# Kernel optimization log

Hardware: AMD Instinct MI355X
Metric: run time of the kernel (lower is better)

Reference implementation:

```python
import jax, jax.numpy as jnp
import numpy as np


def setup_inputs() -> dict:
    key = jax.random.key(0)
    k1, k2 = jax.random.split(key)
    BN, C, P, K = 1024, 3, 128, 15
    patches = jax.random.normal(k1, (BN, C, P, P), dtype=jnp.float32)
    kernels = jax.random.normal(k2, (BN, C, K, K), dtype=jnp.float32)
    return {
        "patches": patches,
        "kernels": kernels,
        "kernel_size": K,
        "patch_size": P,
        "fft_size": 256,  # unused by the spatial-domain path, kept for interface parity
    }


def reference(patches, kernels, kernel_size, patch_size, fft_size):
    # patches: [BN, C, P, P], kernels: [BN, C, K, K] (C == C_k branch of original)
    BN, C, P, _ = patches.shape
    K = kernel_size
    pad = K // 2
    # torch flips the kernel then runs correlation (F.conv2d) -> true convolution
    kf = jnp.flip(kernels, axis=(-2, -1))
    x = patches.reshape(1, BN * C, P, P)          # one big grouped conv
    w = kf.reshape(BN * C, 1, K, K)               # OIHW, one filter per group
    y = jax.lax.conv_general_dilated(
        x, w,
        window_strides=(1, 1),
        padding=[(pad, pad), (pad, pad)],          # zero pad == F.pad + valid conv
        dimension_numbers=("NCHW", "OIHW", "NCHW"),
        feature_group_count=BN * C,
    )
    return y.reshape(BN, C, P, P)
```

## Files before the change

### kernel.cpp

```cpp
#include <hip/hip_runtime.h>


namespace {

constexpr int P      = 128;
constexpr int K      = 15;
constexpr int HALF   = 64;
constexpr int LROWS  = HALF + K - 1;
constexpr int LM     = 36;
constexpr int LWP    = 160;
constexpr int NT     = 256;

__device__ __forceinline__ int dein(int m) {
    return (m >> 1) + (m & 1) * 20;
}

__device__ __forceinline__ int rowkey(int row) {
    return (row >> 1) & 6;
}

__global__ __launch_bounds__(NT, 3)
void dwconv_kernel(const float* __restrict__ patches,
                   const float* __restrict__ kernels,
                   float* __restrict__ out)
{
    __shared__ float xs[LROWS * LWP];

    const int tid   = threadIdx.x;
    const int n     = blockIdx.x >> 1;
    const int halfb = blockIdx.x & 1;
    const int ibase = halfb * HALF;

    const float* img  = patches + (size_t)n * (P * P);
    const float* kern = kernels + (size_t)n * (K * K);

    for (int idx = tid; idx < LROWS * LM; idx += NT) {
        const int row = idx / LM;
        const int m   = idx - row * LM;
        const int r   = ibase - 7 + row;
        const int g0  = m * 4 - 8;
        float4 v = make_float4(0.f, 0.f, 0.f, 0.f);
        if ((unsigned)r < (unsigned)P) {
            if (g0 >= 0 && g0 + 3 < P) {
                v = *reinterpret_cast<const float4*>(img + r * P + g0);
            } else {
                float t0 = 0.f, t1 = 0.f, t2 = 0.f, t3 = 0.f;
                const float* rp = img + r * P;
                if ((unsigned)(g0 + 0) < (unsigned)P) t0 = rp[g0 + 0];
                if ((unsigned)(g0 + 1) < (unsigned)P) t1 = rp[g0 + 1];
                if ((unsigned)(g0 + 2) < (unsigned)P) t2 = rp[g0 + 2];
                if ((unsigned)(g0 + 3) < (unsigned)P) t3 = rp[g0 + 3];
                v = make_float4(t0, t1, t2, t3);
            }
        }
        const int phys = dein(m) ^ rowkey(row);
        *reinterpret_cast<float4*>(xs + row * LWP + 4 * phys) = v;
    }
    __syncthreads();

    const int ty = tid >> 4;
    const int tx = tid & 15;
    const int i0 = ty * 4;
    const int j0 = tx * 8;

    const int dbase[6] = { tx + 0, tx + 20, tx + 1, tx + 21, tx + 2, tx + 22 };

    float acc[4][8];
    #pragma unroll
    for (int rr = 0; rr < 4; ++rr)
        #pragma unroll
        for (int s = 0; s < 8; ++s)
            acc[rr][s] = 0.0f;

    float xw[24];
    float kr[4][K];

    auto loadx = [&](int t) {
        const int lrow = i0 + t;
        const float* xrow = xs + lrow * LWP;
        const int key = rowkey(lrow);
        #pragma unroll
        for (int q = 0; q < 6; ++q) {
            const float4 xv =
                *reinterpret_cast<const float4*>(xrow + 4 * (dbase[q] ^ key));
            xw[q * 4 + 0] = xv.x;
            xw[q * 4 + 1] = xv.y;
            xw[q * 4 + 2] = xv.z;
            xw[q * 4 + 3] = xv.w;
        }
    };

    auto loadk = [&](int slot, int a) {
        #pragma unroll
        for (int b = 0; b < K; ++b) kr[slot][b] = kern[a * K + b];
    };

    auto fmarow = [&](int rr, int slot) {
        #pragma unroll
        for (int b = 0; b < K; ++b)
            #pragma unroll
            for (int s = 0; s < 8; ++s)
                acc[rr][s] = fmaf(xw[s + 15 - b], kr[slot][b], acc[rr][s]);
    };

    loadk(2, 14); loadk(1, 13); loadk(0, 12);
    loadx(0); fmarow(0, 2);
    loadx(1); fmarow(0, 1); fmarow(1, 2);
    loadx(2); fmarow(0, 0); fmarow(1, 1); fmarow(2, 2);

    #pragma unroll 1
    for (int tb = 3; tb <= 14; tb += 4) {
        loadk(3, 14 - tb); loadx(tb + 0);
        fmarow(0, 3); fmarow(1, 0); fmarow(2, 1); fmarow(3, 2);

        loadk(2, 13 - tb); loadx(tb + 1);
        fmarow(0, 2); fmarow(1, 3); fmarow(2, 0); fmarow(3, 1);

        loadk(1, 12 - tb); loadx(tb + 2);
        fmarow(0, 1); fmarow(1, 2); fmarow(2, 3); fmarow(3, 0);

        loadk(0, 11 - tb); loadx(tb + 3);
        fmarow(0, 0); fmarow(1, 1); fmarow(2, 2); fmarow(3, 3);
    }

    loadx(15); fmarow(1, 0); fmarow(2, 1); fmarow(3, 2);
    loadx(16); fmarow(2, 0); fmarow(3, 1);
    loadx(17); fmarow(3, 0);

    float* orow = out + (size_t)n * (P * P) + (size_t)(ibase + i0) * P + j0;
    #pragma unroll
    for (int rr = 0; rr < 4; ++rr) {
        *reinterpret_cast<float4*>(orow + rr * P + 0) =
            make_float4(acc[rr][0], acc[rr][1], acc[rr][2], acc[rr][3]);
        *reinterpret_cast<float4*>(orow + rr * P + 4) =
            make_float4(acc[rr][4], acc[rr][5], acc[rr][6], acc[rr][7]);
    }
}

}

extern "C" void kernel_launch(void* const* d_in, const int* in_sizes, int n_in,
                              void* d_out, int out_size, void* d_ws, size_t ws_size,
                              hipStream_t stream) {
    const float* patches = (const float*)d_in[0];
    const float* kernels = (const float*)d_in[1];
    float* out = (float*)d_out;

    const int n_images = in_sizes[0] / (P * P);
    const int grid = n_images * 2;

    dwconv_kernel<<<grid, NT, 0, stream>>>(patches, kernels, out);
}
```

Baseline: 490.0 us.

## Double-buffer shared-memory row loads and drop XOR swizzle for padded stride

Replaces the XOR row swizzle with a padded row stride (152 floats) to avoid LDS bank conflicts more cheaply. It double-buffers the per-row input window (xwA/xwB), so the next row's LDS loads are issued before the current row's FMAs, hiding LDS latency. The global-to-shared fill loop also swaps per-iteration division for incremental index updates. The extra 24-float buffer raises register pressure, which could cut occupancy under launch_bounds(256,3) or cause spills.

```diff
diff --git a/kernel.cpp b/kernel.cpp
--- a/kernel.cpp
+++ b/kernel.cpp
@@ -8,15 +8,11 @@
 constexpr int HALF   = 64;
 constexpr int LROWS  = HALF + K - 1;
 constexpr int LM     = 36;
-constexpr int LWP    = 160;
+constexpr int LWP    = 152;
 constexpr int NT     = 256;
 
 __device__ __forceinline__ int dein(int m) {
     return (m >> 1) + (m & 1) * 20;
-}
-
-__device__ __forceinline__ int rowkey(int row) {
-    return (row >> 1) & 6;
 }
 
 __global__ __launch_bounds__(NT, 3)
@@ -34,27 +30,30 @@
     const float* img  = patches + (size_t)n * (P * P);
     const float* kern = kernels + (size_t)n * (K * K);
 
-    for (int idx = tid; idx < LROWS * LM; idx += NT) {
-        const int row = idx / LM;
-        const int m   = idx - row * LM;
-        const int r   = ibase - 7 + row;
-        const int g0  = m * 4 - 8;
-        float4 v = make_float4(0.f, 0.f, 0.f, 0.f);
-        if ((unsigned)r < (unsigned)P) {
-            if (g0 >= 0 && g0 + 3 < P) {
-                v = *reinterpret_cast<const float4*>(img + r * P + g0);
-            } else {
-                float t0 = 0.f, t1 = 0.f, t2 = 0.f, t3 = 0.f;
-                const float* rp = img + r * P;
-                if ((unsigned)(g0 + 0) < (unsigned)P) t0 = rp[g0 + 0];
-                if ((unsigned)(g0 + 1) < (unsigned)P) t1 = rp[g0 + 1];
-                if ((unsigned)(g0 + 2) < (unsigned)P) t2 = rp[g0 + 2];
-                if ((unsigned)(g0 + 3) < (unsigned)P) t3 = rp[g0 + 3];
-                v = make_float4(t0, t1, t2, t3);
+    {
+        int row = tid / LM;
+        int m   = tid - row * LM;
+        while (row < LROWS) {
+            const int r  = ibase - 7 + row;
+            const int g0 = m * 4 - 8;
+            float4 v = make_float4(0.f, 0.f, 0.f, 0.f);
+            if ((unsigned)r < (unsigned)P) {
+                if (g0 >= 0 && g0 + 3 < P) {
+                    v = *reinterpret_cast<const float4*>(img + r * P + g0);
+                } else {
+                    float t0 = 0.f, t1 = 0.f, t2 = 0.f, t3 = 0.f;
+                    const float* rp = img + r * P;
+                    if ((unsigned)(g0 + 0) < (unsigned)P) t0 = rp[g0 + 0];
+                    if ((unsigned)(g0 + 1) < (unsigned)P) t1 = rp[g0 + 1];
+                    if ((unsigned)(g0 + 2) < (unsigned)P) t2 = rp[g0 + 2];
+                    if ((unsigned)(g0 + 3) < (unsigned)P) t3 = rp[g0 + 3];
+                    v = make_float4(t0, t1, t2, t3);
+                }
             }
+            *reinterpret_cast<float4*>(xs + row * LWP + 4 * dein(m)) = v;
+            row += 7; m += 4;
+            if (m >= LM) { m -= LM; ++row; }
         }
-        const int phys = dein(m) ^ rowkey(row);
-        *reinterpret_cast<float4*>(xs + row * LWP + 4 * phys) = v;
     }
     __syncthreads();
 
@@ -63,7 +62,7 @@
     const int i0 = ty * 4;
     const int j0 = tx * 8;
 
-    const int dbase[6] = { tx + 0, tx + 20, tx + 1, tx + 21, tx + 2, tx + 22 };
+    const float* xbase = xs + i0 * LWP + 4 * tx;
 
     float acc[4][8];
     #pragma unroll
@@ -72,60 +71,72 @@
         for (int s = 0; s < 8; ++s)
             acc[rr][s] = 0.0f;
 
-    float xw[24];
+    float xwA[24], xwB[24];
     float kr[4][K];
 
-    auto loadx = [&](int t) {
-        const int lrow = i0 + t;
-        const float* xrow = xs + lrow * LWP;
-        const int key = rowkey(lrow);
-        #pragma unroll
-        for (int q = 0; q < 6; ++q) {
-            const float4 xv =
-                *reinterpret_cast<const float4*>(xrow + 4 * (dbase[q] ^ key));
-            xw[q * 4 + 0] = xv.x;
-            xw[q * 4 + 1] = xv.y;
-            xw[q * 4 + 2] = xv.z;
-            xw[q * 4 + 3] = xv.w;
-        }
-    };
+#define LOADX(W, t) do {                                                     \
+        const float* xr_ = xbase + (t) * LWP;                                \
+        const float4 v0_ = *reinterpret_cast<const float4*>(xr_ + 0);        \
+        const float4 v1_ = *reinterpret_cast<const float4*>(xr_ + 80);       \
+        const float4 v2_ = *reinterpret_cast<const float4*>(xr_ + 4);        \
+        const float4 v3_ = *reinterpret_cast<const float4*>(xr_ + 84);       \
+        const float4 v4_ = *reinterpret_cast<const float4*>(xr_ + 8);        \
+        const float4 v5_ = *reinterpret_cast<const float4*>(xr_ + 88);       \
+        W[0]=v0_.x;  W[1]=v0_.y;  W[2]=v0_.z;  W[3]=v0_.w;                   \
+        W[4]=v1_.x;  W[5]=v1_.y;  W[6]=v1_.z;  W[7]=v1_.w;                   \
+        W[8]=v2_.x;  W[9]=v2_.y;  W[10]=v2_.z; W[11]=v2_.w;                  \
+        W[12]=v3_.x; W[13]=v3_.y; W[14]=v3_.z; W[15]=v3_.w;                  \
+        W[16]=v4_.x; W[17]=v4_.y; W[18]=v4_.z; W[19]=v4_.w;                  \
+        W[20]=v5_.x; W[21]=v5_.y; W[22]=v5_.z; W[23]=v5_.w;                  \
+    } while (0)
+
+#define FMAROW(W, rr, slot) do {                                             \
+        _Pragma("unroll")                                                    \
+        for (int b_ = 0; b_ < K; ++b_)                                       \
+            _Pragma("unroll")                                                \
+            for (int s_ = 0; s_ < 8; ++s_)                                   \
+                acc[rr][s_] = fmaf(W[s_ + 15 - b_], kr[slot][b_],            \
+                                   acc[rr][s_]);                             \
+    } while (0)
 
     auto loadk = [&](int slot, int a) {
         #pragma unroll
         for (int b = 0; b < K; ++b) kr[slot][b] = kern[a * K + b];
     };
 
-    auto fmarow = [&](int rr, int slot) {
-        #pragma unroll
-        for (int b = 0; b < K; ++b)
-            #pragma unroll
-            for (int s = 0; s < 8; ++s)
-                acc[rr][s] = fmaf(xw[s + 15 - b], kr[slot][b], acc[rr][s]);
-    };
-
     loadk(2, 14); loadk(1, 13); loadk(0, 12);
-    loadx(0); fmarow(0, 2);
-    loadx(1); fmarow(0, 1); fmarow(1, 2);
-    loadx(2); fmarow(0, 0); fmarow(1, 1); fmarow(2, 2);
+    LOADX(xwA, 0);
+    LOADX(xwB, 1);
+    FMAROW(xwA, 0, 2);
+    LOADX(xwA, 2);
+    FMAROW(xwB, 0, 1); FMAROW(xwB, 1, 2);
+    LOADX(xwB, 3);
+    FMAROW(xwA, 0, 0); FMAROW(xwA, 1, 1); FMAROW(xwA, 2, 2);
 
     #pragma unroll 1
-    for (int tb = 3; tb <= 14; tb += 4) {
-        loadk(3, 14 - tb); loadx(tb + 0);
-        fmarow(0, 3); fmarow(1, 0); fmarow(2, 1); fmarow(3, 2);
-
-        loadk(2, 13 - tb); loadx(tb + 1);
-        fmarow(0, 2); fmarow(1, 3); fmarow(2, 0); fmarow(3, 1);
-
-        loadk(1, 12 - tb); loadx(tb + 2);
-        fmarow(0, 1); fmarow(1, 2); fmarow(2, 3); fmarow(3, 0);
-
-        loadk(0, 11 - tb); loadx(tb + 3);
-        fmarow(0, 0); fmarow(1, 1); fmarow(2, 2); fmarow(3, 3);
+    for (int tb = 3; tb <= 11; tb += 4) {
+        loadk(3, 14 - tb); LOADX(xwA, tb + 1);
+        FMAROW(xwB, 1, 0); FMAROW(xwB, 2, 1); FMAROW(xwB, 3, 2);
+        FMAROW(xwB, 0, 3);
+        loadk(2, 13 - tb); LOADX(xwB, tb + 2);
+        FMAROW(xwA, 1, 3); FMAROW(xwA, 2, 0); FMAROW(xwA, 3, 1);
+        FMAROW(xwA, 0, 2);
+        loadk(1, 12 - tb); LOADX(xwA, tb + 3);
+        FMAROW(xwB, 1, 2); FMAROW(xwB, 2, 3); FMAROW(xwB, 3, 0);
+        FMAROW(xwB, 0, 1);
+        loadk(0, 11 - tb); LOADX(xwB, tb + 4);
+        FMAROW(xwA, 1, 1); FMAROW(xwA, 2, 2); FMAROW(xwA, 3, 3);
+        FMAROW(xwA, 0, 0);
     }
 
-    loadx(15); fmarow(1, 0); fmarow(2, 1); fmarow(3, 2);
-    loadx(16); fmarow(2, 0); fmarow(3, 1);
-    loadx(17); fmarow(3, 0);
+    LOADX(xwA, 16);
+    FMAROW(xwB, 1, 0); FMAROW(xwB, 2, 1); FMAROW(xwB, 3, 2);
+    LOADX(xwB, 17);
+    FMAROW(xwA, 2, 0); FMAROW(xwA, 3, 1);
+    FMAROW(xwB, 3, 0);
+
+#undef LOADX
+#undef FMAROW
 
     float* orow = out + (size_t)n * (P * P) + (size_t)(ibase + i0) * P + j0;
     #pragma unroll
```

Measured after the change: 504.5 us. +3.0%, slower.
